# Optimization experiments

Measured on AMD Instinct MI355X. Metric: run time of the kernel, lower is better.

Reference implementation:

```python
import jax, jax.numpy as jnp
import numpy as np

N_NODES = 40000
N_EDGES = 640000
IN_DIM, H_DIM, OUT_DIM = 128, 128, 64


def setup_inputs() -> dict:
    key = jax.random.key(0)
    ks = jax.random.split(key, 16)
    x = jax.random.normal(ks[0], (N_NODES, IN_DIM), dtype=jnp.float32)
    edge_index = jax.random.randint(ks[1], (2, N_EDGES), 0, N_NODES, dtype=jnp.int64)
    dims = [(IN_DIM, H_DIM), (H_DIM, H_DIM), (H_DIM, OUT_DIM)]
    inp = {"x": x, "edge_index": edge_index}
    for l, (di, do) in enumerate(dims):
        s = 1.0 / np.sqrt(di)
        inp[f"Wr{l}"] = jax.random.uniform(ks[2 + 3 * l], (di, do), jnp.float32, -s, s)  # lin_rel weight
        inp[f"br{l}"] = jax.random.uniform(ks[3 + 3 * l], (do,), jnp.float32, -s, s)     # lin_rel bias
        inp[f"Ws{l}"] = jax.random.uniform(ks[4 + 3 * l], (di, do), jnp.float32, -s, s)  # lin_root weight (no bias)
    return inp


def _graph_conv(x, src, dst, Wr, br, Ws):
    # PyG GraphConv (aggr='add'): out = lin_rel(sum_{j in N(i)} x_j) + lin_root(x_i)
    agg = jax.ops.segment_sum(x[src], dst, num_segments=N_NODES)  # [N, d_in]
    return agg @ Wr + br + x @ Ws


def reference(x, edge_index, Wr0, br0, Ws0, Wr1, br1, Ws1, Wr2, br2, Ws2):
    src, dst = edge_index[0], edge_index[1]
    h = x
    for Wr, br, Ws in ((Wr0, br0, Ws0), (Wr1, br1, Ws1), (Wr2, br2, Ws2)):
        h = _graph_conv(h, src, dst, Wr, br, Ws)
        h = jax.nn.relu(h)
        # dropout p=0 / eval mode -> identity
    return jax.nn.log_softmax(h, axis=1)
```

## Files before the change

### kernel.cpp

```cpp
#include <hip/hip_runtime.h>
#include <hip/hip_bf16.h>


#define N_NODES 40000
#define N_EDGES 640000
#define PAD_NODES 40064
#define DEG_CAP   40960
#define ROW_CAP   64

typedef float v4f __attribute__((ext_vector_type(4)));
typedef float v2f __attribute__((ext_vector_type(2)));
typedef short short8 __attribute__((ext_vector_type(8)));

__device__ inline unsigned short f2b(float f) {
    unsigned u = __float_as_uint(f);
    return (unsigned short)((u + 0x7fffu + ((u >> 16) & 1u)) >> 16);
}

__device__ inline unsigned b2f8(unsigned short us) {
    unsigned s  = ((unsigned)us >> 8) & 0x80u;
    unsigned mag = us & 0x7fffu;
    unsigned e8 = mag >> 7, m7 = mag & 0x7fu;
    unsigned out;
    if (e8 < 121u) out = 0u;
    else if (e8 > 135u) out = 0x7eu;
    else {
        unsigned e4 = e8 - 120u;
        unsigned r  = (m7 + 7u + ((m7 >> 4) & 1u)) >> 4;
        if (r == 8u) { r = 0u; e4++; }
        out = (e4 > 15u || (e4 == 15u && r > 6u)) ? 0x7eu : ((e4 << 3) | r);
    }
    return s | out;
}

__device__ inline unsigned pack4_fp8(float f0, float f1, float f2, float f3) {
#if __has_builtin(__builtin_amdgcn_cvt_pk_fp8_f32)
    int w = __builtin_amdgcn_cvt_pk_fp8_f32(f0, f1, 0, false);
    w = __builtin_amdgcn_cvt_pk_fp8_f32(f2, f3, w, true);
    return (unsigned)w;
#else
    return b2f8(f2b(f0)) | (b2f8(f2b(f1)) << 8) |
           (b2f8(f2b(f2)) << 16) | (b2f8(f2b(f3)) << 24);
#endif
}

#if __has_builtin(__builtin_amdgcn_cvt_f32_fp8)
#define F8TOF(w, sel) __builtin_amdgcn_cvt_f32_fp8((int)(w), (sel))
#else
__device__ inline float f8tof_(unsigned b) {
    unsigned e = (b >> 3) & 15u;
    unsigned bits = ((b & 0x80u) << 24) |
                    (e ? (((e + 120u) << 23) | ((b & 7u) << 20)) : 0u);
    return __uint_as_float(bits);
}
#define F8TOF(w, sel) f8tof_(((unsigned)(w) >> ((sel) * 8)) & 0xffu)
#endif

__global__ __launch_bounds__(256) void prep_kernel(const float* __restrict__ Wr0, const float* __restrict__ Ws0,
                                                   const float* __restrict__ Wr1, const float* __restrict__ Ws1,
                                                   const float* __restrict__ Wr2, const float* __restrict__ Ws2,
                                                   const float* __restrict__ x,
                                                   unsigned short* __restrict__ Wt0,
                                                   unsigned short* __restrict__ Wt1,
                                                   unsigned short* __restrict__ Wt2,
                                                   unsigned short* __restrict__ Xb,
                                                   int* __restrict__ deg) {
    int tid = blockIdx.x * 256 + threadIdx.x;
    if (tid < DEG_CAP / 4) {
        ((int4*)deg)[tid] = make_int4(0, 0, 0, 0);
        return;
    }
    int t = tid - DEG_CAP / 4;
    if (t < 32768) {
        int n = t >> 7, k = t & 127;
        const float* W = (n < 128) ? Wr0 : Ws0;
        Wt0[t] = f2b(W[k * 128 + (n & 127)]);
    } else if (t < 65536) {
        int u = t - 32768;
        int n = u >> 7, k = u & 127;
        const float* W = (n < 128) ? Wr1 : Ws1;
        Wt1[u] = f2b(W[k * 128 + (n & 127)]);
    } else if (t < 81920) {
        int u = t - 65536;
        int n = u >> 7, k = u & 127;
        const float* W = (n < 64) ? Wr2 : Ws2;
        Wt2[u] = f2b(W[k * 64 + (n & 63)]);
    } else {
        int u = t - 81920;
        if (u < (N_NODES * 128) / 8) {
            float4 a = ((const float4*)x)[u * 2];
            float4 b = ((const float4*)x)[u * 2 + 1];
            uint4 o;
            o.x = (unsigned)f2b(a.x) | ((unsigned)f2b(a.y) << 16);
            o.y = (unsigned)f2b(a.z) | ((unsigned)f2b(a.w) << 16);
            o.z = (unsigned)f2b(b.x) | ((unsigned)f2b(b.y) << 16);
            o.w = (unsigned)f2b(b.z) | ((unsigned)f2b(b.w) << 16);
            ((uint4*)Xb)[u] = o;
        }
    }
}

__global__ __launch_bounds__(256) void place_kernel(const int* __restrict__ src,
                                                    const int* __restrict__ dst,
                                                    int* __restrict__ deg,
                                                    int* __restrict__ esrc) {
    int e = blockIdx.x * 256 + threadIdx.x;
    if (e < N_EDGES) {
        int d = dst[e];
        int r = atomicAdd(&deg[d], 1);
        if (r < ROW_CAP) esrc[(size_t)d * ROW_CAP + r] = src[e];
    }
}

template <int DO>
__global__ __launch_bounds__(256, 4) void mm_kernel(const unsigned short* __restrict__ Ab,
                                                    const unsigned short* __restrict__ Wt,
                                                    void* __restrict__ Tout,
                                                    unsigned short* __restrict__ S) {
    __shared__ unsigned short Smem[128 * 128];
    unsigned short* As = Smem;
    unsigned short* Bs = Smem + 128 * 64;

    const int tid = threadIdx.x;
    const int m0  = blockIdx.x * 128;
    const int n0  = blockIdx.y * 128;

    const int wave = tid >> 6;
    const int lane = tid & 63;
    const int wr   = (wave >> 1) * 64;
    const int wc   = (wave & 1) * 64;
    const int qm   = lane & 15;
    const int k8   = (lane >> 4) * 8;

    v4f acc[4][4];
#pragma unroll
    for (int i = 0; i < 4; i++)
#pragma unroll
        for (int j = 0; j < 4; j++) acc[i][j] = (v4f)(0.0f);

#pragma unroll
    for (int half = 0; half < 2; half++) {
#pragma unroll
        for (int i = 0; i < 4; i++) {
            int idx = i * 256 + tid;
            int row = idx >> 3, c8 = idx & 7;
            ((uint4*)As)[idx] =
                *(const uint4*)(Ab + (size_t)(m0 + row) * 128 + half * 64 + c8 * 8);
        }
#pragma unroll
        for (int i = 0; i < 4; i++) {
            int idx = i * 256 + tid;
            int row = idx >> 3, c8 = idx & 7;
            ((uint4*)Bs)[idx] =
                *(const uint4*)(Wt + (size_t)(n0 + row) * 128 + half * 64 + c8 * 8);
        }
        __syncthreads();

#pragma unroll
        for (int ks = 0; ks < 2; ks++) {
            short8 af[4], bf[4];
#pragma unroll
            for (int i = 0; i < 4; i++) {
                af[i] = *(const short8*)(const void*)(As + (wr + i * 16 + qm) * 64 + ks * 32 + k8);
                bf[i] = *(const short8*)(const void*)(Bs + (wc + i * 16 + qm) * 64 + ks * 32 + k8);
            }
#pragma unroll
            for (int mi = 0; mi < 4; mi++)
#pragma unroll
                for (int ni = 0; ni < 4; ni++)
                    acc[mi][ni] = __builtin_amdgcn_mfma_f32_16x16x32_bf16(af[mi], bf[ni], acc[mi][ni], 0, 0, 0);
        }
        __syncthreads();
    }

#pragma unroll
    for (int mi = 0; mi < 4; mi++) {
        const int rowBase = wr + mi * 16 + ((lane >> 4) << 2);
#pragma unroll
        for (int r = 0; r < 4; r++) {
            const int row = rowBase + r;
            const int sw  = ((row >> 2) & 3) << 4;
#pragma unroll
            for (int ni = 0; ni < 4; ni++) {
                const int c = wc + ni * 16 + qm;
                Smem[row * 128 + (c ^ sw)] = f2b(acc[mi][ni][r]);
            }
        }
    }
    __syncthreads();

    if (DO == 128 && n0 == 0) {
        unsigned char* T8 = (unsigned char*)Tout;
#pragma unroll
        for (int i = 0; i < 4; i++) {
            const int chunk = i * 256 + tid;
            const int row   = chunk >> 3;
            const int c0    = (chunk & 7) * 16;
            const int sw    = ((row >> 2) & 3) << 4;
            const int node  = m0 + row;
            if (node <= N_NODES) {
                uint4 v = make_uint4(0, 0, 0, 0);
                if (node < N_NODES) {
                    const unsigned short* p = Smem + row * 128 + (c0 ^ sw);
                    uint4 ha = *(const uint4*)p;
                    uint4 hb = *(const uint4*)(p + 8);
#define LOF(d) __uint_as_float((d) << 16)
#define HIF(d) __uint_as_float((d) & 0xffff0000u)
                    v.x = pack4_fp8(LOF(ha.x), HIF(ha.x), LOF(ha.y), HIF(ha.y));
                    v.y = pack4_fp8(LOF(ha.z), HIF(ha.z), LOF(ha.w), HIF(ha.w));
                    v.z = pack4_fp8(LOF(hb.x), HIF(hb.x), LOF(hb.y), HIF(hb.y));
                    v.w = pack4_fp8(LOF(hb.z), HIF(hb.z), LOF(hb.w), HIF(hb.w));
#undef LOF
#undef HIF
                }
                *(uint4*)(T8 + (size_t)node * 128 + c0) = v;
            }
        }
    } else {
        unsigned short* T = (unsigned short*)Tout;
#pragma unroll
        for (int i = 0; i < 8; i++) {
            const int chunk = i * 256 + tid;
            const int row   = chunk >> 4;
            const int c0    = (chunk & 15) * 8;
            const int sw    = ((row >> 2) & 3) << 4;
            const int node  = m0 + row;
            if (node <= N_NODES) {
                uint4 v = make_uint4(0, 0, 0, 0);
                if (node < N_NODES)
                    v = *(const uint4*)(Smem + row * 128 + (c0 ^ sw));
                if (DO == 128) {
                    *(uint4*)(S + (size_t)node * 128 + c0) = v;
                } else {
                    if (c0 < 64) *(uint4*)(T + (size_t)node * 64 + c0) = v;
                    else         *(uint4*)(S + (size_t)node * 64 + (c0 - 64)) = v;
                }
            }
        }
    }
}

__device__ inline void addp(v2f* a, uint4 q) {
    v2f t0 = { __uint_as_float(q.x << 16), __uint_as_float(q.x & 0xffff0000u) };
    v2f t1 = { __uint_as_float(q.y << 16), __uint_as_float(q.y & 0xffff0000u) };
    v2f t2 = { __uint_as_float(q.z << 16), __uint_as_float(q.z & 0xffff0000u) };
    v2f t3 = { __uint_as_float(q.w << 16), __uint_as_float(q.w & 0xffff0000u) };
    a[0] += t0; a[1] += t1; a[2] += t2; a[3] += t3;
}
__device__ inline void addp8w(v2f* a, unsigned w) {
    v2f t0 = { F8TOF(w, 0), F8TOF(w, 1) };
    v2f t1 = { F8TOF(w, 2), F8TOF(w, 3) };
    a[0] += t0; a[1] += t1;
}
__device__ inline void addp16(v2f* a, uint4 q) {
    addp8w(a + 0, q.x); addp8w(a + 2, q.y);
    addp8w(a + 4, q.z); addp8w(a + 6, q.w);
}

template <int DO, bool LAST, bool FP8T>
__global__ __launch_bounds__(256) void aggregate_kernel(const void* __restrict__ Tin,
                                                        const unsigned short* __restrict__ S,
                                                        const float* __restrict__ br,
                                                        const int* __restrict__ deg,
                                                        const int* __restrict__ esrc,
                                                        unsigned short* __restrict__ Hout,
                                                        float* __restrict__ Fout) {
    constexpr int TPN = 8;
    constexpr int DPL = DO / TPN;
    constexpr int G   = 256 / TPN;
    const int lane = threadIdx.x % TPN;
    const int n    = blockIdx.x * G + threadIdx.x / TPN;

    int cnt = deg[n];
    if (cnt > ROW_CAP) cnt = ROW_CAP;
    const int* erow = esrc + (size_t)n * ROW_CAP;
    const uint4* T4 = (const uint4*)Tin;

    v2f acc[DPL / 2];
#pragma unroll
    for (int i = 0; i < DPL / 2; i++) acc[i] = (v2f)(0.0f);

    for (int o = 0; o < cnt; o += 8) {
        int4 i0 = *(const int4*)(erow + o);
        int4 i1 = *(const int4*)(erow + o + 4);
        i0.x = (o + 0 < cnt) ? i0.x : N_NODES;
        i0.y = (o + 1 < cnt) ? i0.y : N_NODES;
        i0.z = (o + 2 < cnt) ? i0.z : N_NODES;
        i0.w = (o + 3 < cnt) ? i0.w : N_NODES;
        i1.x = (o + 4 < cnt) ? i1.x : N_NODES;
        i1.y = (o + 5 < cnt) ? i1.y : N_NODES;
        i1.z = (o + 6 < cnt) ? i1.z : N_NODES;
        i1.w = (o + 7 < cnt) ? i1.w : N_NODES;
        uint4 q0 = T4[(size_t)i0.x * TPN + lane];
        uint4 q1 = T4[(size_t)i0.y * TPN + lane];
        uint4 q2 = T4[(size_t)i0.z * TPN + lane];
        uint4 q3 = T4[(size_t)i0.w * TPN + lane];
        uint4 q4 = T4[(size_t)i1.x * TPN + lane];
        uint4 q5 = T4[(size_t)i1.y * TPN + lane];
        uint4 q6 = T4[(size_t)i1.z * TPN + lane];
        uint4 q7 = T4[(size_t)i1.w * TPN + lane];
        if (FP8T) {
            addp16(acc, q0); addp16(acc, q1); addp16(acc, q2); addp16(acc, q3);
            addp16(acc, q4); addp16(acc, q5); addp16(acc, q6); addp16(acc, q7);
        } else {
            addp(acc, q0); addp(acc, q1); addp(acc, q2); addp(acc, q3);
            addp(acc, q4); addp(acc, q5); addp(acc, q6); addp(acc, q7);
        }
    }

    float v[DPL];
#pragma unroll
    for (int h = 0; h < DPL / 8; h++) {
        uint4 sv = ((const uint4*)S)[(size_t)n * (DO / 8) + lane * (DPL / 8) + h];
        addp(acc + h * 4, sv);
    }
#pragma unroll
    for (int j = 0; j < DPL; j++) {
        float bj = br[lane * DPL + j];
        v[j] = fmaxf(((j & 1) ? acc[j >> 1].y : acc[j >> 1].x) + bj, 0.f);
    }

    if (LAST) {
        float m = v[0];
#pragma unroll
        for (int i = 1; i < 8; i++) m = fmaxf(m, v[i]);
#pragma unroll
        for (int off = 4; off; off >>= 1) m = fmaxf(m, __shfl_xor(m, off, 64));
        float es = 0.f;
#pragma unroll
        for (int i = 0; i < 8; i++) es += expf(v[i] - m);
#pragma unroll
        for (int off = 4; off; off >>= 1) es += __shfl_xor(es, off, 64);
        float lse = m + logf(es);
        float4 o0 = make_float4(v[0] - lse, v[1] - lse, v[2] - lse, v[3] - lse);
        float4 o1 = make_float4(v[4] - lse, v[5] - lse, v[6] - lse, v[7] - lse);
        ((float4*)Fout)[(size_t)n * 16 + lane * 2]     = o0;
        ((float4*)Fout)[(size_t)n * 16 + lane * 2 + 1] = o1;
    } else {
#pragma unroll
        for (int h = 0; h < DPL / 8; h++) {
            uint4 o;
            o.x = (unsigned)f2b(v[h * 8 + 0]) | ((unsigned)f2b(v[h * 8 + 1]) << 16);
            o.y = (unsigned)f2b(v[h * 8 + 2]) | ((unsigned)f2b(v[h * 8 + 3]) << 16);
            o.z = (unsigned)f2b(v[h * 8 + 4]) | ((unsigned)f2b(v[h * 8 + 5]) << 16);
            o.w = (unsigned)f2b(v[h * 8 + 6]) | ((unsigned)f2b(v[h * 8 + 7]) << 16);
            ((uint4*)Hout)[(size_t)n * (DO / 8) + lane * (DPL / 8) + h] = o;
        }
    }
}


extern "C" void kernel_launch(void* const* d_in, const int* in_sizes, int n_in,
                              void* d_out, int out_size, void* d_ws, size_t ws_size,
                              hipStream_t stream) {
    const float* x    = (const float*)d_in[0];
    const int*   eidx = (const int*)d_in[1];
    const float* Wr0  = (const float*)d_in[2];
    const float* br0  = (const float*)d_in[3];
    const float* Ws0  = (const float*)d_in[4];
    const float* Wr1  = (const float*)d_in[5];
    const float* br1  = (const float*)d_in[6];
    const float* Ws1  = (const float*)d_in[7];
    const float* Wr2  = (const float*)d_in[8];
    const float* br2  = (const float*)d_in[9];
    const float* Ws2  = (const float*)d_in[10];
    float* out = (float*)d_out;

    const int* src = eidx;
    const int* dst = eidx + N_EDGES;

    auto align = [](size_t v) { return (v + 255) & ~(size_t)255; };
    char* w = (char*)d_ws;
    int* deg  = (int*)w;  w += align(sizeof(int) * DEG_CAP);
    int* esrc = (int*)w;  w += align(sizeof(int) * (size_t)N_NODES * ROW_CAP);
    unsigned short* Xb  = (unsigned short*)w;  w += align(2ull * PAD_NODES * 128);
    unsigned short* H1b = (unsigned short*)w;  w += align(2ull * PAD_NODES * 128);
    unsigned short* H2b = (unsigned short*)w;  w += align(2ull * PAD_NODES * 128);
    unsigned short* Wt0 = (unsigned short*)w;  w += align(2ull * 256 * 128);
    unsigned short* Wt1 = (unsigned short*)w;  w += align(2ull * 256 * 128);
    unsigned short* Wt2 = (unsigned short*)w;  w += align(2ull * 128 * 128);
    void*           T   = (void*)w;            w += align(2ull * PAD_NODES * 128);
    unsigned short* Sb  = (unsigned short*)w;  w += align(2ull * PAD_NODES * 128);
    (void)ws_size; (void)n_in; (void)in_sizes; (void)out_size;

    prep_kernel<<<(DEG_CAP / 4 + 81920 + (N_NODES * 128) / 8 + 255) / 256, 256, 0, stream>>>(
        Wr0, Ws0, Wr1, Ws1, Wr2, Ws2, x, Wt0, Wt1, Wt2, Xb, deg);

    place_kernel<<<(N_EDGES + 255) / 256, 256, 0, stream>>>(src, dst, deg, esrc);

    mm_kernel<128><<<dim3(PAD_NODES / 128, 2), 256, 0, stream>>>(Xb, Wt0, T, Sb);
    aggregate_kernel<128, false, true><<<N_NODES / 32, 256, 0, stream>>>(T, Sb, br0, deg, esrc, H1b, nullptr);

    mm_kernel<128><<<dim3(PAD_NODES / 128, 2), 256, 0, stream>>>(H1b, Wt1, T, Sb);
    aggregate_kernel<128, false, true><<<N_NODES / 32, 256, 0, stream>>>(T, Sb, br1, deg, esrc, H2b, nullptr);

    mm_kernel<64><<<dim3(PAD_NODES / 128, 1), 256, 0, stream>>>(H2b, Wt2, T, Sb);
    aggregate_kernel<64, true, false><<<N_NODES / 32, 256, 0, stream>>>(T, Sb, br2, deg, esrc, nullptr, out);
}
```

Measured before the change: 203.3 us.

## Halve GEMM row tile and split neighbor gather across two thread groups per node

The GEMM kernel now uses 64-row tiles with each wave covering 32 output columns, which halves shared memory and raises the occupancy hint so more blocks run concurrently. The aggregate kernel assigns 16 threads per node instead of 8, with two groups taking alternating chunks of 8 edges and combining partial sums through a shuffle. The aim is more memory-level parallelism in the latency-bound neighbor gather and better GPU fill. The cost is a doubled grid, an extra reduction step, and half the threads idle during output writes.

```diff
diff --git a/kernel.cpp b/kernel.cpp
--- a/kernel.cpp
+++ b/kernel.cpp
@@ -113,35 +113,34 @@
 }
 
 template <int DO>
-__global__ __launch_bounds__(256, 4) void mm_kernel(const unsigned short* __restrict__ Ab,
+__global__ __launch_bounds__(256, 6) void mm_kernel(const unsigned short* __restrict__ Ab,
                                                     const unsigned short* __restrict__ Wt,
                                                     void* __restrict__ Tout,
                                                     unsigned short* __restrict__ S) {
-    __shared__ unsigned short Smem[128 * 128];
+    __shared__ unsigned short Smem[64 * 64 + 128 * 64];
     unsigned short* As = Smem;
-    unsigned short* Bs = Smem + 128 * 64;
+    unsigned short* Bs = Smem + 64 * 64;
 
     const int tid = threadIdx.x;
-    const int m0  = blockIdx.x * 128;
+    const int m0  = blockIdx.x * 64;
     const int n0  = blockIdx.y * 128;
 
     const int wave = tid >> 6;
     const int lane = tid & 63;
-    const int wr   = (wave >> 1) * 64;
-    const int wc   = (wave & 1) * 64;
+    const int wc   = wave * 32;
     const int qm   = lane & 15;
     const int k8   = (lane >> 4) * 8;
 
-    v4f acc[4][4];
+    v4f acc[4][2];
 #pragma unroll
     for (int i = 0; i < 4; i++)
 #pragma unroll
-        for (int j = 0; j < 4; j++) acc[i][j] = (v4f)(0.0f);
+        for (int j = 0; j < 2; j++) acc[i][j] = (v4f)(0.0f);
 
 #pragma unroll
     for (int half = 0; half < 2; half++) {
 #pragma unroll
-        for (int i = 0; i < 4; i++) {
+        for (int i = 0; i < 2; i++) {
             int idx = i * 256 + tid;
             int row = idx >> 3, c8 = idx & 7;
             ((uint4*)As)[idx] =
@@ -158,16 +157,17 @@
 
 #pragma unroll
         for (int ks = 0; ks < 2; ks++) {
-            short8 af[4], bf[4];
-#pragma unroll
-            for (int i = 0; i < 4; i++) {
-                af[i] = *(const short8*)(const void*)(As + (wr + i * 16 + qm) * 64 + ks * 32 + k8);
-                bf[i] = *(const short8*)(const void*)(Bs + (wc + i * 16 + qm) * 64 + ks * 32 + k8);
-            }
+            short8 af[4], bf[2];
+#pragma unroll
+            for (int i = 0; i < 4; i++)
+                af[i] = *(const short8*)(const void*)(As + (i * 16 + qm) * 64 + ks * 32 + k8);
+#pragma unroll
+            for (int j = 0; j < 2; j++)
+                bf[j] = *(const short8*)(const void*)(Bs + (wc + j * 16 + qm) * 64 + ks * 32 + k8);
 #pragma unroll
             for (int mi = 0; mi < 4; mi++)
 #pragma unroll
-                for (int ni = 0; ni < 4; ni++)
+                for (int ni = 0; ni < 2; ni++)
                     acc[mi][ni] = __builtin_amdgcn_mfma_f32_16x16x32_bf16(af[mi], bf[ni], acc[mi][ni], 0, 0, 0);
         }
         __syncthreads();
@@ -175,13 +175,13 @@
 
 #pragma unroll
     for (int mi = 0; mi < 4; mi++) {
-        const int rowBase = wr + mi * 16 + ((lane >> 4) << 2);
+        const int rowBase = mi * 16 + ((lane >> 4) << 2);
 #pragma unroll
         for (int r = 0; r < 4; r++) {
             const int row = rowBase + r;
             const int sw  = ((row >> 2) & 3) << 4;
 #pragma unroll
-            for (int ni = 0; ni < 4; ni++) {
+            for (int ni = 0; ni < 2; ni++) {
                 const int c = wc + ni * 16 + qm;
                 Smem[row * 128 + (c ^ sw)] = f2b(acc[mi][ni][r]);
             }
@@ -192,7 +192,7 @@
     if (DO == 128 && n0 == 0) {
         unsigned char* T8 = (unsigned char*)Tout;
 #pragma unroll
-        for (int i = 0; i < 4; i++) {
+        for (int i = 0; i < 2; i++) {
             const int chunk = i * 256 + tid;
             const int row   = chunk >> 3;
             const int c0    = (chunk & 7) * 16;
@@ -219,7 +219,7 @@
     } else {
         unsigned short* T = (unsigned short*)Tout;
 #pragma unroll
-        for (int i = 0; i < 8; i++) {
+        for (int i = 0; i < 4; i++) {
             const int chunk = i * 256 + tid;
             const int row   = chunk >> 4;
             const int c0    = (chunk & 15) * 8;
@@ -265,11 +265,11 @@
                                                         const int* __restrict__ esrc,
                                                         unsigned short* __restrict__ Hout,
                                                         float* __restrict__ Fout) {
-    constexpr int TPN = 8;
-    constexpr int DPL = DO / TPN;
-    constexpr int G   = 256 / TPN;
-    const int lane = threadIdx.x % TPN;
-    const int n    = blockIdx.x * G + threadIdx.x / TPN;
+    constexpr int DPL = FP8T ? 16 : 8;
+    const int lane16 = threadIdx.x & 15;
+    const int g      = lane16 >> 3;
+    const int lane   = lane16 & 7;
+    const int n      = blockIdx.x * 16 + (threadIdx.x >> 4);
 
     int cnt = deg[n];
     if (cnt > ROW_CAP) cnt = ROW_CAP;
@@ -280,7 +280,7 @@
 #pragma unroll
     for (int i = 0; i < DPL / 2; i++) acc[i] = (v2f)(0.0f);
 
-    for (int o = 0; o < cnt; o += 8) {
+    for (int o = g * 8; o < cnt; o += 16) {
         int4 i0 = *(const int4*)(erow + o);
         int4 i1 = *(const int4*)(erow + o + 4);
         i0.x = (o + 0 < cnt) ? i0.x : N_NODES;
@@ -291,14 +291,14 @@
         i1.y = (o + 5 < cnt) ? i1.y : N_NODES;
         i1.z = (o + 6 < cnt) ? i1.z : N_NODES;
         i1.w = (o + 7 < cnt) ? i1.w : N_NODES;
-        uint4 q0 = T4[(size_t)i0.x * TPN + lane];
-        uint4 q1 = T4[(size_t)i0.y * TPN + lane];
-        uint4 q2 = T4[(size_t)i0.z * TPN + lane];
-        uint4 q3 = T4[(size_t)i0.w * TPN + lane];
-        uint4 q4 = T4[(size_t)i1.x * TPN + lane];
-        uint4 q5 = T4[(size_t)i1.y * TPN + lane];
-        uint4 q6 = T4[(size_t)i1.z * TPN + lane];
-        uint4 q7 = T4[(size_t)i1.w * TPN + lane];
+        uint4 q0 = T4[(size_t)i0.x * 8 + lane];
+        uint4 q1 = T4[(size_t)i0.y * 8 + lane];
+        uint4 q2 = T4[(size_t)i0.z * 8 + lane];
+        uint4 q3 = T4[(size_t)i0.w * 8 + lane];
+        uint4 q4 = T4[(size_t)i1.x * 8 + lane];
+        uint4 q5 = T4[(size_t)i1.y * 8 + lane];
+        uint4 q6 = T4[(size_t)i1.z * 8 + lane];
+        uint4 q7 = T4[(size_t)i1.w * 8 + lane];
         if (FP8T) {
             addp16(acc, q0); addp16(acc, q1); addp16(acc, q2); addp16(acc, q3);
             addp16(acc, q4); addp16(acc, q5); addp16(acc, q6); addp16(acc, q7);
@@ -308,6 +308,12 @@
         }
     }
 
+#pragma unroll
+    for (int i = 0; i < DPL / 2; i++) {
+        acc[i].x += __shfl_xor(acc[i].x, 8);
+        acc[i].y += __shfl_xor(acc[i].y, 8);
+    }
+
     float v[DPL];
 #pragma unroll
     for (int h = 0; h < DPL / 8; h++) {
@@ -325,18 +331,20 @@
 #pragma unroll
         for (int i = 1; i < 8; i++) m = fmaxf(m, v[i]);
 #pragma unroll
-        for (int off = 4; off; off >>= 1) m = fmaxf(m, __shfl_xor(m, off, 64));
+        for (int off = 4; off; off >>= 1) m = fmaxf(m, __shfl_xor(m, off));
         float es = 0.f;
 #pragma unroll
         for (int i = 0; i < 8; i++) es += expf(v[i] - m);
 #pragma unroll
-        for (int off = 4; off; off >>= 1) es += __shfl_xor(es, off, 64);
+        for (int off = 4; off; off >>= 1) es += __shfl_xor(es, off);
         float lse = m + logf(es);
-        float4 o0 = make_float4(v[0] - lse, v[1] - lse, v[2] - lse, v[3] - lse);
-        float4 o1 = make_float4(v[4] - lse, v[5] - lse, v[6] - lse, v[7] - lse);
-        ((float4*)Fout)[(size_t)n * 16 + lane * 2]     = o0;
-        ((float4*)Fout)[(size_t)n * 16 + lane * 2 + 1] = o1;
-    } else {
+        if (g == 0) {
+            float4 o0 = make_float4(v[0] - lse, v[1] - lse, v[2] - lse, v[3] - lse);
+            float4 o1 = make_float4(v[4] - lse, v[5] - lse, v[6] - lse, v[7] - lse);
+            ((float4*)Fout)[(size_t)n * 16 + lane * 2]     = o0;
+            ((float4*)Fout)[(size_t)n * 16 + lane * 2 + 1] = o1;
+        }
+    } else if (g == 0) {
 #pragma unroll
         for (int h = 0; h < DPL / 8; h++) {
             uint4 o;
@@ -388,12 +396,12 @@
 
     place_kernel<<<(N_EDGES + 255) / 256, 256, 0, stream>>>(src, dst, deg, esrc);
 
-    mm_kernel<128><<<dim3(PAD_NODES / 128, 2), 256, 0, stream>>>(Xb, Wt0, T, Sb);
-    aggregate_kernel<128, false, true><<<N_NODES / 32, 256, 0, stream>>>(T, Sb, br0, deg, esrc, H1b, nullptr);
-
-    mm_kernel<128><<<dim3(PAD_NODES / 128, 2), 256, 0, stream>>>(H1b, Wt1, T, Sb);
-    aggregate_kernel<128, false, true><<<N_NODES / 32, 256, 0, stream>>>(T, Sb, br1, deg, esrc, H2b, nullptr);
-
-    mm_kernel<64><<<dim3(PAD_NODES / 128, 1), 256, 0, stream>>>(H2b, Wt2, T, Sb);
-    aggregate_kernel<64, true, false><<<N_NODES / 32, 256, 0, stream>>>(T, Sb, br2, deg, esrc, nullptr, out);
-}
+    mm_kernel<128><<<dim3(PAD_NODES / 64, 2), 256, 0, stream>>>(Xb, Wt0, T, Sb);
+    aggregate_kernel<128, false, true><<<N_NODES / 16, 256, 0, stream>>>(T, Sb, br0, deg, esrc, H1b, nullptr);
+
+    mm_kernel<128><<<dim3(PAD_NODES / 64, 2), 256, 0, stream>>>(H1b, Wt1, T, Sb);
+    aggregate_kernel<128, false, true><<<N_NODES / 16, 256, 0, stream>>>(T, Sb, br1, deg, esrc, H2b, nullptr);
+
+    mm_kernel<64><<<dim3(PAD_NODES / 64, 1), 256, 0, stream>>>(H2b, Wt2, T, Sb);
+    aggregate_kernel<64, true, false><<<N_NODES / 16, 256, 0, stream>>>(T, Sb, br2, deg, esrc, nullptr, out);
+}
```

Measured after the change: 199.5 us. About the same (-1.9%).
